# Kernel optimization log

Measured on AMD Instinct MI355X. Metric: run time of the kernel, lower is better.

The kernel has to match this reference:

```python
import jax, jax.numpy as jnp
import numpy as np

FIN, FOUT, FH, LAT = 64, 64, 128, 512
B, H, Wd = 16, 128, 128
SIZES = [FH * FIN, FH * FH, FH * FH, FOUT * FH, FOUT * FIN, FH, FH, FH, FOUT, FOUT]
KTOT = sum(SIZES)


def setup_inputs() -> dict:
    key = jax.random.key(0)
    k1, k2, k3, k4 = jax.random.split(key, 4)
    x = jax.random.normal(k1, (B, FIN, H, Wd), dtype=jnp.float32)
    lat = jax.random.normal(k2, (B, LAT), dtype=jnp.float32)
    W = jax.random.normal(k3, (KTOT, LAT), dtype=jnp.float32) * 0.02
    b = jax.random.normal(k4, (KTOT,), dtype=jnp.float32) * 0.02
    return {"x": x, "lat": lat, "W": W, "b": b}


def _split_kernels(ks):
    # ks: [B, KTOT] hypernetwork output -> per-sample 1x1 conv weights + biases
    offs = np.cumsum([0] + SIZES)
    parts = [ks[:, offs[i]:offs[i + 1]] for i in range(10)]
    k_in = parts[0].reshape(B, FH, FIN) / jnp.sqrt(FH)
    k_mida = parts[1].reshape(B, FH, FH) / jnp.sqrt(FH)
    k_midb = parts[2].reshape(B, FH, FH) / jnp.sqrt(FH)
    k_out = parts[3].reshape(B, FOUT, FH) / jnp.sqrt(FOUT)
    k_short = parts[4].reshape(B, FOUT, FIN) / jnp.sqrt(FOUT)
    b_in = parts[5].reshape(B, FH, 1, 1)
    b_mida = parts[6].reshape(B, FH, 1, 1)
    b_midb = parts[7].reshape(B, FH, 1, 1)
    b_out = parts[8].reshape(B, FOUT, 1, 1)
    b_short = parts[9].reshape(B, FOUT, 1, 1)
    return k_in, k_mida, k_midb, k_out, k_short, b_in, b_mida, b_midb, b_out, b_short


def _pconv(k, xv):
    # per-sample 1x1 conv: k [B,O,I], xv [B,I,H,W] -> [B,O,H,W]
    return jnp.einsum('boi,bihw->bohw', k, xv)


def reference(x, lat, W, b):
    ks = lat @ W.T + b  # [B, KTOT]
    k_in, k_mida, k_midb, k_out, k_short, b_in, b_mida, b_midb, b_out, b_short = _split_kernels(ks)
    x_s = _pconv(k_short, x) + b_short
    h = jax.nn.relu(_pconv(k_in, x) + b_in)
    h = jax.nn.relu(_pconv(k_mida, h) + b_mida)
    h = jax.nn.relu(_pconv(k_midb, h) + b_midb)
    out = _pconv(k_out, h) + b_out + x_s
    return out
```

## Files before the change

### kernel.cpp

```cpp
#include <hip/hip_runtime.h>
#include <cstdint>
#include <cstddef>


typedef short bf16x8 __attribute__((ext_vector_type(8)));
typedef float f32x4  __attribute__((ext_vector_type(4)));
typedef float f32x16 __attribute__((ext_vector_type(16)));

#define DEVFN static __device__ __forceinline__

constexpr int WELEM      = 53248;
constexpr size_t WS_WSHORTS = (size_t)WELEM;
constexpr size_t WS_WBYTES_TOT = (size_t)16 * WELEM * 2;
constexpr size_t WS_BOFF  = WS_WBYTES_TOT;
constexpr size_t WS_AHOFF = WS_BOFF + 16 * 512 * 4;
constexpr size_t WS_ALOFF = WS_AHOFF + 16384;

DEVFN unsigned bf16rne(float f) {
  unsigned u = __builtin_bit_cast(unsigned, f);
  return (u + 0x7fffu + ((u >> 16) & 1u)) >> 16;
}
DEVFN unsigned pk2(float lo, float hi) {
  return bf16rne(lo) | (bf16rne(hi) << 16);
}

__global__ __launch_bounds__(256) void lat_prep(
    const float* __restrict__ lat, unsigned short* __restrict__ ah_ws,
    unsigned short* __restrict__ al_ws) {
  const int id = blockIdx.x * 256 + threadIdx.x;
  const int s = id >> 6, l = id & 63;
  const int m = l & 15, q = l >> 4;
  const float* ap = lat + m * 512 + s * 32 + q * 8;
  float f[8];
#pragma unroll
  for (int j = 0; j < 8; ++j) f[j] = ap[j];
  unsigned H[4], L[4];
#pragma unroll
  for (int p = 0; p < 4; ++p) {
    const unsigned u0 = __builtin_bit_cast(unsigned, f[2 * p]);
    const unsigned u1 = __builtin_bit_cast(unsigned, f[2 * p + 1]);
    const unsigned h0 = u0 & 0xFFFF0000u, h1 = u1 & 0xFFFF0000u;
    H[p] = (h0 >> 16) | h1;
    const float lo0 = f[2 * p] - __builtin_bit_cast(float, h0);
    const float lo1 = f[2 * p + 1] - __builtin_bit_cast(float, h1);
    L[p] = pk2(lo0, lo1);
  }
  *(uint4*)&ah_ws[(size_t)(s * 64 + l) * 8] = make_uint4(H[0], H[1], H[2], H[3]);
  *(uint4*)&al_ws[(size_t)(s * 64 + l) * 8] = make_uint4(L[0], L[1], L[2], L[3]);
}

#define MFMA16(A, B, C) __builtin_amdgcn_mfma_f32_16x16x32_bf16((A), (B), (C), 0, 0, 0)

__global__ __launch_bounds__(256, 2) void hyper_gemm(
    const float* __restrict__ W, const float* __restrict__ bias,
    const unsigned short* __restrict__ ah_ws,
    const unsigned short* __restrict__ al_ws,
    unsigned short* __restrict__ w_ws, float* __restrict__ b_ws) {
  const int tid = threadIdx.x;
  const int wv = tid >> 6;
  const int l = tid & 63;
  const int q = l >> 4;
  const int g = blockIdx.x * 4 + wv;
  const int n0 = g * 16;
  const int n = n0 + (l & 15);

  bf16x8 Ah[16], Al[16];
#pragma unroll
  for (int s = 0; s < 16; ++s) {
    Ah[s] = *(const bf16x8*)&ah_ws[(size_t)(s * 64 + l) * 8];
    Al[s] = *(const bf16x8*)&al_ws[(size_t)(s * 64 + l) * 8];
  }

  const float* bp = W + (size_t)n * 512 + q * 8;
  float4 ld[8][2];
#pragma unroll
  for (int s = 0; s < 8; ++s) {
    ld[s][0] = *(const float4*)(bp + s * 32);
    ld[s][1] = *(const float4*)(bp + s * 32 + 4);
  }

  f32x4 acc = {0.f, 0.f, 0.f, 0.f};
#pragma unroll
  for (int s = 0; s < 16; ++s) {
    const float4 b0 = ld[s & 7][0];
    const float4 b1 = ld[s & 7][1];
    if (s < 8) {
      ld[s][0] = *(const float4*)(bp + (s + 8) * 32);
      ld[s][1] = *(const float4*)(bp + (s + 8) * 32 + 4);
    }
    const float f[8] = {b0.x, b0.y, b0.z, b0.w, b1.x, b1.y, b1.z, b1.w};
    union { unsigned u[4]; bf16x8 v; } BH, BL;
#pragma unroll
    for (int p = 0; p < 4; ++p) {
      const unsigned u0 = __builtin_bit_cast(unsigned, f[2 * p]);
      const unsigned u1 = __builtin_bit_cast(unsigned, f[2 * p + 1]);
      const unsigned h0 = u0 & 0xFFFF0000u, h1 = u1 & 0xFFFF0000u;
      BH.u[p] = (h0 >> 16) | h1;
      const float lo0 = f[2 * p] - __builtin_bit_cast(float, h0);
      const float lo1 = f[2 * p + 1] - __builtin_bit_cast(float, h1);
      BL.u[p] = pk2(lo0, lo1);
    }
    acc = MFMA16(Ah[s], BH.v, acc);
    acc = MFMA16(Ah[s], BL.v, acc);
    acc = MFMA16(Al[s], BH.v, acc);
  }

  const float bv = bias[n];
  if (n0 >= 53248) {
    const int j = n - 53248;
#pragma unroll
    for (int r = 0; r < 4; ++r) b_ws[(q * 4 + r) * 512 + j] = acc[r] + bv;
    return;
  }
  int fragbase, off, kbits;
  float scale;
  if (n < 8192)       { fragbase = 0;  off = 0;     kbits = 6; scale = 0.08838834764831845f; }
  else if (n < 24576) { fragbase = 16; off = 8192;  kbits = 7; scale = 0.08838834764831845f; }
  else if (n < 40960) { fragbase = 48; off = 24576; kbits = 7; scale = 0.08838834764831845f; }
  else if (n < 49152) { fragbase = 80; off = 40960; kbits = 7; scale = 0.125f; }
  else                { fragbase = 96; off = 49152; kbits = 6; scale = 0.125f; }
  const int r0 = n - off;
  const int m = r0 >> kbits;
  const int k = r0 & ((1 << kbits) - 1);
  const int mt = m >> 5, ks = k >> 4;
  const int lane = (m & 31) + 32 * ((k >> 3) & 1);
  const int j = k & 7;
  const int frag = fragbase + mt * (1 << (kbits - 4)) + ks;
  const size_t eoff = (size_t)frag * 512 + lane * 8 + j;
#pragma unroll
  for (int r = 0; r < 4; ++r) {
    const float v = (acc[r] + bv) * scale;
    w_ws[(size_t)(q * 4 + r) * WS_WSHORTS + eoff] = (unsigned short)bf16rne(v);
  }
}


DEVFN f32x16 bias_init(const float* bl, int mt, int lh) {
  f32x16 a;
#pragma unroll
  for (int g = 0; g < 4; ++g) {
    const float4 bv = *(const float4*)&bl[mt * 32 + 8 * g + 4 * lh];
    a[4 * g + 0] = bv.x; a[4 * g + 1] = bv.y;
    a[4 * g + 2] = bv.z; a[4 * g + 3] = bv.w;
  }
  return a;
}

DEVFN void write_h(short* hb, int mt, int l31, int lh, const f32x16& a0,
                   const f32x16& a1) {
#pragma unroll
  for (int g = 0; g < 4; ++g) {
    const int kstep = mt * 2 + (g >> 1);
    const int sub = g & 1;
    const int base = (kstep * 2) * 512 + (l31 + 32 * sub) * 8 + lh * 4;
    uint2 w0, w1;
    w0.x = pk2(fmaxf(a0[4 * g + 0], 0.f), fmaxf(a0[4 * g + 1], 0.f));
    w0.y = pk2(fmaxf(a0[4 * g + 2], 0.f), fmaxf(a0[4 * g + 3], 0.f));
    w1.x = pk2(fmaxf(a1[4 * g + 0], 0.f), fmaxf(a1[4 * g + 1], 0.f));
    w1.y = pk2(fmaxf(a1[4 * g + 2], 0.f), fmaxf(a1[4 * g + 3], 0.f));
    *(uint2*)&hb[base] = w0;
    *(uint2*)&hb[base + 512] = w1;
  }
}

#define MFMA32(A, B, C) __builtin_amdgcn_mfma_f32_32x32x16_bf16((A), (B), (C), 0, 0, 0)

__global__ __launch_bounds__(256, 1) void dyn_conv(
    const float* __restrict__ x, const unsigned short* __restrict__ w_ws,
    const float* __restrict__ b_ws, float* __restrict__ out) {
  __shared__ short wl[72 * 512];
  __shared__ float bl[512];
  __shared__ short hl[4][8192];

  const int s = blockIdx.x >> 4;
  const int chunk = blockIdx.x & 15;
  const int tid = threadIdx.x;
  const int wv = tid >> 6;
  const int l = tid & 63;
  const int l31 = l & 31;
  const int lh = l >> 5;

  const unsigned short* wbase = w_ws + (size_t)s * WS_WSHORTS;

  for (int f = wv; f < 72; f += 4) {
    const int fg = (f < 16) ? f : f + 32;
    *(int4*)&wl[f * 512 + l * 8] = *(const int4*)&wbase[fg * 512 + l * 8];
  }
  bl[tid] = b_ws[s * 512 + tid];
  bl[tid + 256] = b_ws[s * 512 + tid + 256];

  bf16x8 Am[32];
#pragma unroll
  for (int i = 0; i < 32; ++i)
    Am[i] = *(const bf16x8*)&wbase[(16 + i) * 512 + l * 8];

  const float* xbase = x + (size_t)(s * 64) * 16384;
  float xr[2][4][8];
  auto load_xr = [&](int it) {
    const int px0 = chunk * 1024 + it * 256 + wv * 64;
#pragma unroll
    for (int nt = 0; nt < 2; ++nt) {
#pragma unroll
      for (int ks = 0; ks < 4; ++ks) {
        const float* xp =
            xbase + (size_t)(ks * 16 + lh * 8) * 16384 + px0 + nt * 32 + l31;
#pragma unroll
        for (int j = 0; j < 8; ++j) xr[nt][ks][j] = xp[(size_t)j * 16384];
      }
    }
  };
  load_xr(0);

  __syncthreads();

  short* hb = &hl[wv][0];

#pragma unroll 1
  for (int it = 0; it < 4; ++it) {
    const int px0 = chunk * 1024 + it * 256 + wv * 64;

    bf16x8 xf[2][4];
#pragma unroll
    for (int nt = 0; nt < 2; ++nt) {
#pragma unroll
      for (int ks = 0; ks < 4; ++ks) {
        union { unsigned u[4]; bf16x8 v8; } uu;
#pragma unroll
        for (int j = 0; j < 4; ++j)
          uu.u[j] = pk2(xr[nt][ks][2 * j], xr[nt][ks][2 * j + 1]);
        xf[nt][ks] = uu.v8;
      }
    }
    if (it < 3) load_xr(it + 1);

#pragma unroll
    for (int mt = 0; mt < 4; ++mt) {
      f32x16 a0 = bias_init(bl + 0, mt, lh);
      f32x16 a1 = a0;
#pragma unroll
      for (int ks = 0; ks < 4; ++ks) {
        const bf16x8 A = *(const bf16x8*)&wl[(mt * 4 + ks) * 512 + l * 8];
        a0 = MFMA32(A, xf[0][ks], a0);
        a1 = MFMA32(A, xf[1][ks], a1);
      }
      write_h(hb, mt, l31, lh, a0, a1);
    }

    bf16x8 hB[16];

#pragma unroll
    for (int i = 0; i < 16; ++i) hB[i] = *(const bf16x8*)&hb[i * 512 + l * 8];
#pragma unroll
    for (int mt = 0; mt < 4; ++mt) {
      f32x16 a0 = bias_init(bl + 128, mt, lh);
      f32x16 a1 = a0;
#pragma unroll
      for (int ks = 0; ks < 8; ++ks) {
        a0 = MFMA32(Am[mt * 8 + ks], hB[ks * 2 + 0], a0);
        a1 = MFMA32(Am[mt * 8 + ks], hB[ks * 2 + 1], a1);
      }
      write_h(hb, mt, l31, lh, a0, a1);
    }

#pragma unroll
    for (int i = 0; i < 16; ++i) hB[i] = *(const bf16x8*)&hb[i * 512 + l * 8];
#pragma unroll
    for (int mt = 0; mt < 4; ++mt) {
      f32x16 a0 = bias_init(bl + 256, mt, lh);
      f32x16 a1 = a0;
#pragma unroll
      for (int ks = 0; ks < 8; ++ks) {
        const bf16x8 A = *(const bf16x8*)&wl[(16 + mt * 8 + ks) * 512 + l * 8];
        a0 = MFMA32(A, hB[ks * 2 + 0], a0);
        a1 = MFMA32(A, hB[ks * 2 + 1], a1);
      }
      write_h(hb, mt, l31, lh, a0, a1);
    }

#pragma unroll
    for (int i = 0; i < 16; ++i) hB[i] = *(const bf16x8*)&hb[i * 512 + l * 8];
#pragma unroll
    for (int mt = 0; mt < 2; ++mt) {
      f32x16 a0 = bias_init(bl + 384, mt, lh);
      {
        const f32x16 bs = bias_init(bl + 448, mt, lh);
#pragma unroll
        for (int e = 0; e < 16; ++e) a0[e] += bs[e];
      }
      f32x16 a1 = a0;
#pragma unroll
      for (int ks = 0; ks < 4; ++ks) {
        const bf16x8 A = *(const bf16x8*)&wl[(64 + mt * 4 + ks) * 512 + l * 8];
        a0 = MFMA32(A, xf[0][ks], a0);
        a1 = MFMA32(A, xf[1][ks], a1);
      }
#pragma unroll
      for (int ks = 0; ks < 8; ++ks) {
        const bf16x8 A = *(const bf16x8*)&wl[(48 + mt * 8 + ks) * 512 + l * 8];
        a0 = MFMA32(A, hB[ks * 2 + 0], a0);
        a1 = MFMA32(A, hB[ks * 2 + 1], a1);
      }
#pragma unroll
      for (int g = 0; g < 4; ++g) {
#pragma unroll
        for (int q = 0; q < 4; ++q) {
          const int row = mt * 32 + 8 * g + 4 * lh + q;
          float* op = out + (size_t)(s * 64 + row) * 16384 + px0 + l31;
          op[0]  = a0[4 * g + q];
          op[32] = a1[4 * g + q];
        }
      }
    }
  }
}

extern "C" void kernel_launch(void* const* d_in, const int* in_sizes, int n_in,
                              void* d_out, int out_size, void* d_ws,
                              size_t ws_size, hipStream_t stream) {
  (void)in_sizes; (void)n_in; (void)out_size; (void)ws_size;
  const float* x   = (const float*)d_in[0];
  const float* lat = (const float*)d_in[1];
  const float* W   = (const float*)d_in[2];
  const float* b   = (const float*)d_in[3];
  unsigned short* w_ws = (unsigned short*)d_ws;
  float* b_ws = (float*)((char*)d_ws + WS_BOFF);
  unsigned short* ah_ws = (unsigned short*)((char*)d_ws + WS_AHOFF);
  unsigned short* al_ws = (unsigned short*)((char*)d_ws + WS_ALOFF);
  float* out = (float*)d_out;

  lat_prep<<<dim3(4), dim3(256), 0, stream>>>(lat, ah_ws, al_ws);
  hyper_gemm<<<dim3(840), dim3(256), 0, stream>>>(W, b, ah_ws, al_ws, w_ws, b_ws);
  dyn_conv<<<dim3(256), dim3(256), 0, stream>>>(x, w_ws, b_ws, out);
}
```

Before: 267.4 us.

## Keep hidden activations in registers via permlane32 swaps and widen blocks to 512 threads

Intermediate ReLU activations no longer round-trip through per-wave LDS buffers. Accumulator outputs are repacked directly into MFMA B-operand fragments with permlane32_swap. All five weight matrices now go into LDS instead of keeping one in registers, and blocks grow to 8 waves covering 512 pixels per iteration with two blocks per CU. This removes LDS write/read traffic and register pressure from the held weights, at the cost of a larger LDS footprint and a shallower x prefetch.

```diff
diff --git a/kernel.cpp b/kernel.cpp
--- a/kernel.cpp
+++ b/kernel.cpp
@@ -146,31 +146,37 @@
   return a;
 }
 
-DEVFN void write_h(short* hb, int mt, int l31, int lh, const f32x16& a0,
-                   const f32x16& a1) {
+DEVFN void acc_to_bfrags(const f32x16& a0, const f32x16& a1, bf16x8* h, int mt) {
+  unsigned P0[4][2], P1[4][2];
 #pragma unroll
   for (int g = 0; g < 4; ++g) {
-    const int kstep = mt * 2 + (g >> 1);
-    const int sub = g & 1;
-    const int base = (kstep * 2) * 512 + (l31 + 32 * sub) * 8 + lh * 4;
-    uint2 w0, w1;
-    w0.x = pk2(fmaxf(a0[4 * g + 0], 0.f), fmaxf(a0[4 * g + 1], 0.f));
-    w0.y = pk2(fmaxf(a0[4 * g + 2], 0.f), fmaxf(a0[4 * g + 3], 0.f));
-    w1.x = pk2(fmaxf(a1[4 * g + 0], 0.f), fmaxf(a1[4 * g + 1], 0.f));
-    w1.y = pk2(fmaxf(a1[4 * g + 2], 0.f), fmaxf(a1[4 * g + 3], 0.f));
-    *(uint2*)&hb[base] = w0;
-    *(uint2*)&hb[base + 512] = w1;
+    P0[g][0] = pk2(fmaxf(a0[4 * g + 0], 0.f), fmaxf(a0[4 * g + 1], 0.f));
+    P0[g][1] = pk2(fmaxf(a0[4 * g + 2], 0.f), fmaxf(a0[4 * g + 3], 0.f));
+    P1[g][0] = pk2(fmaxf(a1[4 * g + 0], 0.f), fmaxf(a1[4 * g + 1], 0.f));
+    P1[g][1] = pk2(fmaxf(a1[4 * g + 2], 0.f), fmaxf(a1[4 * g + 3], 0.f));
+  }
+#pragma unroll
+  for (int e = 0; e < 2; ++e) {
+    auto r0 = __builtin_amdgcn_permlane32_swap(P0[2 * e][0], P0[2 * e + 1][0], false, false);
+    auto r1 = __builtin_amdgcn_permlane32_swap(P0[2 * e][1], P0[2 * e + 1][1], false, false);
+    union { unsigned u[4]; bf16x8 v; } F0;
+    F0.u[0] = r0[0]; F0.u[1] = r1[0]; F0.u[2] = r0[1]; F0.u[3] = r1[1];
+    h[(2 * mt + e) * 2 + 0] = F0.v;
+    auto q0 = __builtin_amdgcn_permlane32_swap(P1[2 * e][0], P1[2 * e + 1][0], false, false);
+    auto q1 = __builtin_amdgcn_permlane32_swap(P1[2 * e][1], P1[2 * e + 1][1], false, false);
+    union { unsigned u[4]; bf16x8 v; } F1;
+    F1.u[0] = q0[0]; F1.u[1] = q1[0]; F1.u[2] = q0[1]; F1.u[3] = q1[1];
+    h[(2 * mt + e) * 2 + 1] = F1.v;
   }
 }
 
 #define MFMA32(A, B, C) __builtin_amdgcn_mfma_f32_32x32x16_bf16((A), (B), (C), 0, 0, 0)
 
-__global__ __launch_bounds__(256, 1) void dyn_conv(
+__global__ __launch_bounds__(512, 2) void dyn_conv(
     const float* __restrict__ x, const unsigned short* __restrict__ w_ws,
     const float* __restrict__ b_ws, float* __restrict__ out) {
-  __shared__ short wl[72 * 512];
+  __shared__ short wl[104 * 512];
   __shared__ float bl[512];
-  __shared__ short hl[4][8192];
 
   const int s = blockIdx.x >> 4;
   const int chunk = blockIdx.x & 15;
@@ -181,23 +187,11 @@
   const int lh = l >> 5;
 
   const unsigned short* wbase = w_ws + (size_t)s * WS_WSHORTS;
-
-  for (int f = wv; f < 72; f += 4) {
-    const int fg = (f < 16) ? f : f + 32;
-    *(int4*)&wl[f * 512 + l * 8] = *(const int4*)&wbase[fg * 512 + l * 8];
-  }
-  bl[tid] = b_ws[s * 512 + tid];
-  bl[tid + 256] = b_ws[s * 512 + tid + 256];
-
-  bf16x8 Am[32];
-#pragma unroll
-  for (int i = 0; i < 32; ++i)
-    Am[i] = *(const bf16x8*)&wbase[(16 + i) * 512 + l * 8];
-
   const float* xbase = x + (size_t)(s * 64) * 16384;
+
   float xr[2][4][8];
-  auto load_xr = [&](int it) {
-    const int px0 = chunk * 1024 + it * 256 + wv * 64;
+  auto load_xr = [&](int it2) {
+    const int px0 = chunk * 1024 + it2 * 512 + wv * 64;
 #pragma unroll
     for (int nt = 0; nt < 2; ++nt) {
 #pragma unroll
@@ -211,13 +205,15 @@
   };
   load_xr(0);
 
+  for (int f = wv; f < 104; f += 8)
+    *(int4*)&wl[f * 512 + l * 8] = *(const int4*)&wbase[(size_t)f * 512 + l * 8];
+  bl[tid] = b_ws[s * 512 + tid];
+
   __syncthreads();
 
-  short* hb = &hl[wv][0];
-
 #pragma unroll 1
-  for (int it = 0; it < 4; ++it) {
-    const int px0 = chunk * 1024 + it * 256 + wv * 64;
+  for (int it = 0; it < 2; ++it) {
+    const int px0 = chunk * 1024 + it * 512 + wv * 64;
 
     bf16x8 xf[2][4];
 #pragma unroll
@@ -231,7 +227,8 @@
         xf[nt][ks] = uu.v8;
       }
     }
-    if (it < 3) load_xr(it + 1);
+
+    bf16x8 hA[16], hB2[16];
 
 #pragma unroll
     for (int mt = 0; mt < 4; ++mt) {
@@ -243,42 +240,36 @@
         a0 = MFMA32(A, xf[0][ks], a0);
         a1 = MFMA32(A, xf[1][ks], a1);
       }
-      write_h(hb, mt, l31, lh, a0, a1);
-    }
-
-    bf16x8 hB[16];
-
-#pragma unroll
-    for (int i = 0; i < 16; ++i) hB[i] = *(const bf16x8*)&hb[i * 512 + l * 8];
+      acc_to_bfrags(a0, a1, hA, mt);
+    }
+
 #pragma unroll
     for (int mt = 0; mt < 4; ++mt) {
       f32x16 a0 = bias_init(bl + 128, mt, lh);
       f32x16 a1 = a0;
 #pragma unroll
       for (int ks = 0; ks < 8; ++ks) {
-        a0 = MFMA32(Am[mt * 8 + ks], hB[ks * 2 + 0], a0);
-        a1 = MFMA32(Am[mt * 8 + ks], hB[ks * 2 + 1], a1);
-      }
-      write_h(hb, mt, l31, lh, a0, a1);
-    }
-
-#pragma unroll
-    for (int i = 0; i < 16; ++i) hB[i] = *(const bf16x8*)&hb[i * 512 + l * 8];
+        const bf16x8 A = *(const bf16x8*)&wl[(16 + mt * 8 + ks) * 512 + l * 8];
+        a0 = MFMA32(A, hA[ks * 2 + 0], a0);
+        a1 = MFMA32(A, hA[ks * 2 + 1], a1);
+      }
+      acc_to_bfrags(a0, a1, hB2, mt);
+    }
+
 #pragma unroll
     for (int mt = 0; mt < 4; ++mt) {
       f32x16 a0 = bias_init(bl + 256, mt, lh);
       f32x16 a1 = a0;
 #pragma unroll
       for (int ks = 0; ks < 8; ++ks) {
-        const bf16x8 A = *(const bf16x8*)&wl[(16 + mt * 8 + ks) * 512 + l * 8];
-        a0 = MFMA32(A, hB[ks * 2 + 0], a0);
-        a1 = MFMA32(A, hB[ks * 2 + 1], a1);
-      }
-      write_h(hb, mt, l31, lh, a0, a1);
-    }
-
-#pragma unroll
-    for (int i = 0; i < 16; ++i) hB[i] = *(const bf16x8*)&hb[i * 512 + l * 8];
+        const bf16x8 A = *(const bf16x8*)&wl[(48 + mt * 8 + ks) * 512 + l * 8];
+        a0 = MFMA32(A, hB2[ks * 2 + 0], a0);
+        a1 = MFMA32(A, hB2[ks * 2 + 1], a1);
+      }
+      acc_to_bfrags(a0, a1, hA, mt);
+    }
+
+    if (it == 0) load_xr(1);
 #pragma unroll
     for (int mt = 0; mt < 2; ++mt) {
       f32x16 a0 = bias_init(bl + 384, mt, lh);
@@ -290,15 +281,15 @@
       f32x16 a1 = a0;
 #pragma unroll
       for (int ks = 0; ks < 4; ++ks) {
-        const bf16x8 A = *(const bf16x8*)&wl[(64 + mt * 4 + ks) * 512 + l * 8];
+        const bf16x8 A = *(const bf16x8*)&wl[(96 + mt * 4 + ks) * 512 + l * 8];
         a0 = MFMA32(A, xf[0][ks], a0);
         a1 = MFMA32(A, xf[1][ks], a1);
       }
 #pragma unroll
       for (int ks = 0; ks < 8; ++ks) {
-        const bf16x8 A = *(const bf16x8*)&wl[(48 + mt * 8 + ks) * 512 + l * 8];
-        a0 = MFMA32(A, hB[ks * 2 + 0], a0);
-        a1 = MFMA32(A, hB[ks * 2 + 1], a1);
+        const bf16x8 A = *(const bf16x8*)&wl[(80 + mt * 8 + ks) * 512 + l * 8];
+        a0 = MFMA32(A, hA[ks * 2 + 0], a0);
+        a1 = MFMA32(A, hA[ks * 2 + 1], a1);
       }
 #pragma unroll
       for (int g = 0; g < 4; ++g) {
@@ -330,5 +321,5 @@
 
   lat_prep<<<dim3(4), dim3(256), 0, stream>>>(lat, ah_ws, al_ws);
   hyper_gemm<<<dim3(840), dim3(256), 0, stream>>>(W, b, ah_ws, al_ws, w_ws, b_ws);
-  dyn_conv<<<dim3(256), dim3(256), 0, stream>>>(x, w_ws, b_ws, out);
-}
+  dyn_conv<<<dim3(256), dim3(512), 0, stream>>>(x, w_ws, b_ws, out);
+}
```

New measurement: 600.5 us. 125% more time.
